# Performance work log

Measured on AMD Instinct MI355X. Metric: run time of the kernel, lower is better.

The kernel has to match this reference:

```python
import jax, jax.numpy as jnp
import numpy as np

B, S = 2, 2048
H = 16
NOPE, ROPE, VD = 128, 64, 128
Q_RANK, KV_RANK = 1536, 512
SCALE = 1.0 / np.sqrt(NOPE + ROPE)  # 1/sqrt(192)
NEG_INF = -10000.0


def _make_rope(n_pos, dim):
    # matches gen_rope: theta over even indices, angles repeated twice (rotate-half layout)
    theta = 1.0 / (10000.0 ** (np.arange(0, dim, 2, dtype=np.float32) / dim))
    pos = np.arange(n_pos, dtype=np.float32)
    ang = np.outer(pos, theta)                      # [N, dim/2]
    ang = np.concatenate([ang, ang], axis=-1)       # [N, dim]
    return jnp.asarray(np.cos(ang)), jnp.asarray(np.sin(ang))


def _rope(x, cos, sin):
    # rotate-half RoPE; cos/sin broadcast over head dim if present
    d = x.shape[-1]
    x1, x2 = x[..., : d // 2], x[..., d // 2 :]
    rot = jnp.concatenate([-x2, x1], axis=-1)
    return x * cos + rot * sin


def setup_inputs() -> dict:
    key = jax.random.key(0)
    ks = jax.random.split(key, 5)
    Q = jax.random.normal(ks[0], (B, S, Q_RANK), dtype=jnp.float32)
    KV = jax.random.normal(ks[1], (B, S, KV_RANK), dtype=jnp.float32)
    PE = jax.random.normal(ks[2], (B, S, ROPE), dtype=jnp.float32)
    WUQ = jax.random.normal(ks[3], (H * (NOPE + ROPE), Q_RANK), dtype=jnp.float32) * 0.02
    WUKV = jax.random.normal(ks[4], (H * (NOPE + VD), KV_RANK), dtype=jnp.float32) * 0.02
    cos, sin = _make_rope(B * S, ROPE)
    cos = cos.reshape(B, S, ROPE)
    sin = sin.reshape(B, S, ROPE)
    mask = jnp.triu(jnp.full((S, S), NEG_INF, dtype=jnp.float32), k=1)
    return {"Q": Q, "KV": KV, "PE": PE, "WUQ": WUQ, "WUKV": WUKV,
            "cos": cos, "sin": sin, "mask": mask}


def reference(Q, KV, PE, WUQ, WUKV, cos, sin, mask):
    b, s, _ = Q.shape
    # low-rank up-projections
    q = jnp.einsum("bsl,dl->bsd", Q, WUQ).reshape(b, s, H, NOPE + ROPE)
    q_nope, q_pe = q[..., :NOPE], q[..., NOPE:]
    q_pe = _rope(q_pe, cos[:, :, None, :], sin[:, :, None, :])

    kv = jnp.einsum("bsl,dl->bsd", KV, WUKV).reshape(b, s, H, NOPE + VD)
    k_nope, v = kv[..., :NOPE], kv[..., NOPE:]
    k_pe = _rope(PE, cos, sin)  # [b, s, ROPE], shared across heads

    # attention scores: per-head nope part + shared rope part
    scores = jnp.einsum("bqhd,bkhd->bhqk", q_nope, k_nope)
    scores = scores + jnp.einsum("bqhd,bkd->bhqk", q_pe, k_pe)
    scores = scores * SCALE + mask[None, None, :, :]
    attn = jax.nn.softmax(scores, axis=-1)
    out = jnp.einsum("bhqk,bkhd->bqhd", attn, v)  # [b, s, H, VD]
    return out
```

## Files before the change

### kernel.cpp

```cpp
#include <hip/hip_runtime.h>

typedef __attribute__((ext_vector_type(8))) short short8;
typedef __attribute__((ext_vector_type(4))) float f32x4;

#define SS 2048
#define HH 16
#define NOPE_D 128
#define ROPE_D 64
#define VDIM 128
#define QD 192
#define SCALE_F 0.07216878364870323f
#define LOG2E 1.4426950408889634f

__device__ __forceinline__ unsigned short f2bf(float f) {
    unsigned int x = __builtin_bit_cast(unsigned int, f);
    unsigned int r = (x + 0x7fffu + ((x >> 16) & 1u)) >> 16;
    return (unsigned short)r;
}

#define GLDS16(g, l) __builtin_amdgcn_global_load_lds( \
    (const __attribute__((address_space(1))) void*)(g), \
    (__attribute__((address_space(3))) void*)(l), 16, 0, 0)

__global__ __launch_bounds__(256) void cvt_all(
    const float* __restrict__ Q, const float* __restrict__ WUQ,
    const float* __restrict__ KV, const float* __restrict__ WUKV,
    const float* __restrict__ PE, const float* __restrict__ cs, const float* __restrict__ sn,
    unsigned short* __restrict__ Qb, unsigned short* __restrict__ WUQb,
    unsigned short* __restrict__ KVb, unsigned short* __restrict__ WUKVb,
    unsigned short* __restrict__ kpe)
{
    int bid = blockIdx.x;
    if (bid >= 14848) {
        int idx = (bid - 14848) * 256 + threadIdx.x;
        int i = idx & 31, row = idx >> 5;
        float x1 = PE[row * 64 + i], x2 = PE[row * 64 + 32 + i];
        float c1 = cs[row * 64 + i],      s1 = sn[row * 64 + i];
        float c2 = cs[row * 64 + 32 + i], s2 = sn[row * 64 + 32 + i];
        kpe[row * 64 + i]      = f2bf(x1 * c1 - x2 * s1);
        kpe[row * 64 + 32 + i] = f2bf(x2 * c2 + x1 * s2);
        return;
    }
    const float* src; unsigned short* dst; float scale = 1.0f;
    if (bid < 6144)       { src = Q;    dst = Qb; }
    else if (bid < 10752) { src = WUQ;  dst = WUQb; bid -= 6144; scale = SCALE_F * LOG2E; }
    else if (bid < 12800) { src = KV;   dst = KVb;  bid -= 10752; }
    else                  { src = WUKV; dst = WUKVb; bid -= 12800; }
    int i = (bid * 256 + threadIdx.x) * 4;
    float4 v = *(const float4*)(src + i);
    ushort4 o = { f2bf(v.x * scale), f2bf(v.y * scale), f2bf(v.z * scale), f2bf(v.w * scale) };
    *(ushort4*)(dst + i) = o;
}

__global__ __launch_bounds__(256) void gemm_fused(
    const unsigned short* __restrict__ Qb, const unsigned short* __restrict__ WUQb,
    const unsigned short* __restrict__ KVb, const unsigned short* __restrict__ WUKVb,
    unsigned short* __restrict__ qbuf, unsigned short* __restrict__ knope,
    unsigned short* __restrict__ vT,
    const float* __restrict__ cs, const float* __restrict__ sn)
{
    __shared__ unsigned short As[128 * 64];
    __shared__ unsigned short Bs[128 * 64];
    const int t = threadIdx.x, w = t >> 6, lane = t & 63;
    const int n16 = lane & 15, quad = lane >> 4;

    int bid = blockIdx.x;
    const unsigned short *A, *B; int N, K, bm, bn; bool g1;
    if (bid < 768) { g1 = true;  A = Qb;  B = WUQb;  N = 3072; K = 1536;
                     bm = (bid / 24) * 128; bn = (bid % 24) * 128; }
    else           { g1 = false; bid -= 768; A = KVb; B = WUKVb; N = 4096; K = 512;
                     bm = (bid / 32) * 128; bn = (bid % 32) * 128; }

    const int wm = (w >> 1) * 64, wn = (w & 1) * 64;
    f32x4 acc[4][4] = {};

    const int lr = lane >> 3, lc = lane & 7;
    const int sw = (lc ^ lr) * 8;
    const unsigned short* gA = A + (size_t)(bm + w * 32 + lr) * K + sw;
    const unsigned short* gB = B + (size_t)(bn + w * 32 + lr) * K + sw;

    for (int k0 = 0; k0 < K; k0 += 64) {
        __syncthreads();
        for (int j = 0; j < 4; j++) {
            GLDS16(gA + (size_t)j * 8 * K + k0, &As[(w * 32 + j * 8) * 64]);
            GLDS16(gB + (size_t)j * 8 * K + k0, &Bs[(w * 32 + j * 8) * 64]);
        }
        __syncthreads();
        for (int ks = 0; ks < 2; ks++) {
            short8 af[4], bf[4];
            for (int mt = 0; mt < 4; mt++) {
                int rw = wm + mt * 16 + n16;
                af[mt] = *(const short8*)&As[rw * 64 + (((ks * 4 + quad) ^ (rw & 7)) * 8)];
            }
            for (int nt = 0; nt < 4; nt++) {
                int rw = wn + nt * 16 + n16;
                bf[nt] = *(const short8*)&Bs[rw * 64 + (((ks * 4 + quad) ^ (rw & 7)) * 8)];
            }
            for (int mt = 0; mt < 4; mt++)
                for (int nt = 0; nt < 4; nt++)
                    acc[mt][nt] = __builtin_amdgcn_mfma_f32_16x16x32_bf16(af[mt], bf[nt], acc[mt][nt], 0, 0, 0);
        }
    }

    const int colbase = bn + wn;
    if (g1) {
        const bool is_pe = ((colbase % 192) >= 128);
        if (is_pe) {
            for (int mt = 0; mt < 4; mt++)
                for (int r = 0; r < 4; r++) {
                    int row = bm + wm + mt * 16 + quad * 4 + r;
                    const float* cr = cs + row * 64;
                    const float* sr = sn + row * 64;
                    for (int nt = 0; nt < 2; nt++) {
                        int i = nt * 16 + n16;
                        float x1 = acc[mt][nt][r], x2 = acc[mt][nt + 2][r];
                        float o1 = x1 * cr[i] - x2 * sr[i];
                        float o2 = x2 * cr[32 + i] + x1 * sr[32 + i];
                        qbuf[(size_t)row * N + colbase + i] = f2bf(o1);
                        qbuf[(size_t)row * N + colbase + 32 + i] = f2bf(o2);
                    }
                }
        } else {
            for (int mt = 0; mt < 4; mt++)
                for (int nt = 0; nt < 4; nt++)
                    for (int r = 0; r < 4; r++)
                        qbuf[(size_t)(bm + wm + mt * 16 + quad * 4 + r) * N + colbase + nt * 16 + n16]
                            = f2bf(acc[mt][nt][r]);
        }
    } else {
        if ((colbase & 255) < 128) {
            for (int mt = 0; mt < 4; mt++)
                for (int nt = 0; nt < 4; nt++) {
                    int col = colbase + nt * 16 + n16;
                    int h = col >> 8, d = col & 255;
                    for (int r = 0; r < 4; r++)
                        knope[(size_t)(bm + wm + mt * 16 + quad * 4 + r) * 2048 + h * 128 + d]
                            = f2bf(acc[mt][nt][r]);
                }
        } else {
            for (int mt = 0; mt < 4; mt++)
                for (int nt = 0; nt < 4; nt++) {
                    int col = colbase + nt * 16 + n16;
                    int h = col >> 8, vd = (col & 255) - 128;
                    int row0 = bm + wm + mt * 16 + quad * 4;
                    int b = row0 >> 11, s0 = row0 & 2047;
                    int l6 = s0 & 63;
                    int scol = (s0 & ~63) + ((l6 >> 5) & 1) * 32 + ((l6 >> 2) & 3) * 8
                             + ((l6 >> 4) & 1) * 4 + (l6 & 3);
                    ushort4 pk = { f2bf(acc[mt][nt][0]), f2bf(acc[mt][nt][1]),
                                   f2bf(acc[mt][nt][2]), f2bf(acc[mt][nt][3]) };
                    *(ushort4*)&vT[((size_t)(b * 16 + h) * 128 + vd) * 2048 + scol] = pk;
                }
        }
    }
}

#define STAGE(bufsel, kt_) do { \
    int r_ = w * 16 + (lane >> 4), sl_ = lane & 15; \
    for (int j = 0; j < 4; j++) { \
        int rr_ = r_ + j * 4; \
        GLDS16(knb + (size_t)((kt_) * 64 + rr_) * 2048 + ((sl_ ^ (rr_ & 7)) * 8), \
               &Kn[bufsel][(w * 16 + j * 4) * 128]); \
    } \
    int rp_ = w * 16 + (lane >> 3), slp_ = lane & 7; \
    for (int j = 0; j < 2; j++) { \
        int rr_ = rp_ + j * 8; \
        GLDS16(kpb + (size_t)((kt_) * 64 + rr_) * 64 + ((slp_ ^ (rr_ & 7)) * 8), \
               &Kp[bufsel][(w * 16 + j * 8) * 64]); \
    } \
    int r2_ = w * 32 + (lane >> 3), sl2_ = lane & 7; \
    for (int j = 0; j < 4; j++) { \
        int rr_ = r2_ + j * 8; \
        GLDS16(vtb + (size_t)rr_ * 2048 + (kt_) * 64 + ((sl2_ ^ (rr_ & 7)) * 8), \
               &Vt[bufsel][(w * 32 + j * 8) * 64]); \
    } \
} while (0)

#define COMPUTE(bufsel, kt_) do { \
    f32x4 Sg[2][4]; \
    __builtin_amdgcn_s_setprio(1); \
    for (int nt = 0; nt < 4; nt++) { \
        int key = nt * 16 + n16, kx = key & 7; \
        f32x4 a0 = {}, a1 = {}; \
        for (int ks = 0; ks < 4; ks++) { \
            short8 af = *(const short8*)&Kn[bufsel][key * 128 + (((ks * 4 + quad) ^ kx) * 8)]; \
            a0 = __builtin_amdgcn_mfma_f32_16x16x32_bf16(af, qf[0][ks], a0, 0, 0, 0); \
            a1 = __builtin_amdgcn_mfma_f32_16x16x32_bf16(af, qf[1][ks], a1, 0, 0, 0); \
        } \
        for (int ks = 0; ks < 2; ks++) { \
            short8 af = *(const short8*)&Kp[bufsel][key * 64 + (((ks * 4 + quad) ^ kx) * 8)]; \
            a0 = __builtin_amdgcn_mfma_f32_16x16x32_bf16(af, qf[0][4 + ks], a0, 0, 0, 0); \
            a1 = __builtin_amdgcn_mfma_f32_16x16x32_bf16(af, qf[1][4 + ks], a1, 0, 0, 0); \
        } \
        Sg[0][nt] = a0; Sg[1][nt] = a1; \
    } \
    __builtin_amdgcn_s_setprio(0); \
    if ((kt_) >= 2 * qt) {    \
        for (int qg = 0; qg < 2; qg++) { \
            int qq = qt * 128 + w * 32 + qg * 16 + n16; \
            for (int nt = 0; nt < 4; nt++) { \
                int key0 = (kt_) * 64 + nt * 16 + quad * 4; \
                for (int r = 0; r < 4; r++) \
                    if (key0 + r > qq) Sg[qg][nt][r] = -INFINITY; \
            } \
        } \
    } \
     \
    float alpha[2]; \
    for (int qg = 0; qg < 2; qg++) { \
        float mx = -INFINITY; \
        for (int nt = 0; nt < 4; nt++) \
            for (int r = 0; r < 4; r++) mx = fmaxf(mx, Sg[qg][nt][r]); \
        mx = fmaxf(mx, __shfl_xor(mx, 16, 64)); \
        mx = fmaxf(mx, __shfl_xor(mx, 32, 64)); \
        float mnew = fmaxf(m_i[qg], mx); \
        alpha[qg] = exp2f(m_i[qg] - mnew); \
        m_i[qg] = mnew; \
        float rs = 0.f; \
        for (int nt = 0; nt < 4; nt++) \
            for (int r = 0; r < 4; r++) { \
                float pv = exp2f(Sg[qg][nt][r] - mnew); \
                Sg[qg][nt][r] = pv; \
                rs += pv; \
            } \
        l_i[qg] = l_i[qg] * alpha[qg] + rs; \
    } \
     \
     \
    f32x4 av0, av1; \
    for (int r_ = 0; r_ < 4; r_++) { \
        av0[r_] = __shfl(alpha[0], quad * 4 + r_, 64); \
        av1[r_] = __shfl(alpha[1], quad * 4 + r_, 64); \
    } \
    for (int v8 = 0; v8 < 8; v8++) \
        for (int r = 0; r < 4; r++) { \
            O[0][v8][r] *= av0[r]; \
            O[1][v8][r] *= av1[r]; \
        } \
     \
    short8 pp[2][2]; \
    for (int qg = 0; qg < 2; qg++) \
        for (int ntp = 0; ntp < 2; ntp++) { \
            short8 pa; \
            for (int j = 0; j < 4; j++) pa[j] = (short)f2bf(Sg[qg][ntp * 2][j]); \
            for (int j = 0; j < 4; j++) pa[4 + j] = (short)f2bf(Sg[qg][ntp * 2 + 1][j]); \
            pp[qg][ntp] = pa; \
        } \
    __builtin_amdgcn_s_setprio(1); \
    for (int ntp = 0; ntp < 2; ntp++) \
        for (int v8 = 0; v8 < 8; v8++) { \
            int vd = v8 * 16 + n16; \
            short8 vb = *(const short8*)&Vt[bufsel][vd * 64 + (((ntp * 4 + quad) ^ (vd & 7)) * 8)]; \
            O[0][v8] = __builtin_amdgcn_mfma_f32_16x16x32_bf16(pp[0][ntp], vb, O[0][v8], 0, 0, 0); \
            O[1][v8] = __builtin_amdgcn_mfma_f32_16x16x32_bf16(pp[1][ntp], vb, O[1][v8], 0, 0, 0); \
        } \
    __builtin_amdgcn_s_setprio(0); \
} while (0)

__global__ __launch_bounds__(256, 2) void attn_kernel(
    const unsigned short* __restrict__ qbuf,
    const unsigned short* __restrict__ knope,
    const unsigned short* __restrict__ kpe,
    const unsigned short* __restrict__ vT,
    float* __restrict__ out)
{
    const int t = threadIdx.x, w = t >> 6, lane = t & 63;
    const int n16 = lane & 15, quad = lane >> 4;

    __shared__ unsigned short Kn[2][64 * 128];
    __shared__ unsigned short Kp[2][64 * 64];
    __shared__ unsigned short Vt[2][128 * 64];

    const int u = blockIdx.x;
    const int sbits = (u >> 1) & 15;
    const int flip  = (u & 1) ^ ((u >> 8) & 1);
    const int qt = flip ? 15 - sbits : sbits;
    const int c  = ((u >> 5) & 7) | ((u & 1) << 3) | (((u >> 8) & 1) << 4);
    const int h = c & 15, b = c >> 4;

    const unsigned short* knb = knope + (size_t)b * 2048 * 2048 + h * 128;
    const unsigned short* kpb = kpe + (size_t)b * 2048 * 64;
    const unsigned short* vtb = vT + (size_t)(b * 16 + h) * 128 * 2048;

    short8 qf[2][6];
    for (int qg = 0; qg < 2; qg++) {
        size_t grow = (size_t)(b * SS + qt * 128 + w * 32 + qg * 16 + n16);
        const unsigned short* qp = qbuf + grow * (HH * QD) + h * QD + quad * 8;
        for (int ks = 0; ks < 6; ks++) qf[qg][ks] = *(const short8*)(qp + ks * 32);
    }

    f32x4 O[2][8] = {};
    float m_i[2] = { -INFINITY, -INFINITY };
    float l_i[2] = { 0.f, 0.f };

    const int nkt = 2 * qt + 2;

    STAGE(0, 0);
    __syncthreads();
    for (int kt2 = 0; kt2 < nkt; kt2 += 2) {
        STAGE(1, kt2 + 1);
        COMPUTE(0, kt2);
        __syncthreads();
        if (kt2 + 2 < nkt) STAGE(0, kt2 + 2);
        COMPUTE(1, kt2 + 1);
        __syncthreads();
    }

    float l0 = l_i[0];
    l0 += __shfl_xor(l0, 16, 64); l0 += __shfl_xor(l0, 32, 64);
    float l1 = l_i[1];
    l1 += __shfl_xor(l1, 16, 64); l1 += __shfl_xor(l1, 32, 64);
    float rl0 = 1.f / l0, rl1 = 1.f / l1;
    f32x4 lv0, lv1;
    for (int r_ = 0; r_ < 4; r_++) {
        lv0[r_] = __shfl(rl0, quad * 4 + r_, 64);
        lv1[r_] = __shfl(rl1, quad * 4 + r_, 64);
    }
    for (int qg = 0; qg < 2; qg++) {
        const f32x4 lv = qg ? lv1 : lv0;
        for (int r = 0; r < 4; r++) {
            size_t qrow = (size_t)(b * SS + qt * 128 + w * 32 + qg * 16 + quad * 4 + r);
            float* op = out + (qrow * HH + h) * VDIM;
            for (int v8 = 0; v8 < 8; v8++)
                op[v8 * 16 + n16] = O[qg][v8][r] * lv[r];
        }
    }
}

extern "C" void kernel_launch(void* const* d_in, const int* in_sizes, int n_in,
                              void* d_out, int out_size, void* d_ws, size_t ws_size,
                              hipStream_t stream) {
    const float* Q    = (const float*)d_in[0];
    const float* KV   = (const float*)d_in[1];
    const float* PE   = (const float*)d_in[2];
    const float* WUQ  = (const float*)d_in[3];
    const float* WUKV = (const float*)d_in[4];
    const float* cosp = (const float*)d_in[5];
    const float* sinp = (const float*)d_in[6];
    float* out = (float*)d_out;

    unsigned short* qbuf  = (unsigned short*)d_ws;
    unsigned short* knope = qbuf  + (size_t)4096 * 3072;
    unsigned short* vT    = knope + (size_t)4096 * 2048;
    unsigned short* kpe   = vT    + (size_t)4096 * 2048;
    unsigned short* Qb    = kpe   + (size_t)4096 * 64;
    unsigned short* WUQb  = Qb    + (size_t)4096 * 1536;
    unsigned short* KVb   = WUQb  + (size_t)3072 * 1536;
    unsigned short* WUKVb = KVb   + (size_t)4096 * 512;

    cvt_all<<<15360, 256, 0, stream>>>(Q, WUQ, KV, WUKV, PE, cosp, sinp,
                                       Qb, WUQb, KVb, WUKVb, kpe);
    gemm_fused<<<1792, 256, 0, stream>>>(Qb, WUQb, KVb, WUKVb,
                                         qbuf, knope, vT, cosp, sinp);
    attn_kernel<<<512, 256, 0, stream>>>(qbuf, knope, kpe, vT, out);
}
```

Measured before the change: 345.8 us.

## Use partial vmcnt waits, lazy softmax rescaling, and drop setprio and occupancy hint

Replaces the full __syncthreads barriers with explicit s_waitcnt vmcnt(10)/lgkmcnt(0) plus s_barrier, so the next tile's global-to-LDS loads can stay in flight while the current tile is computed. Adds a lazy online-softmax rescale: when every lane's new row max exceeds the running max by at most 8 (log2 domain), the max is not updated and the O rescale is skipped. Also removes the s_setprio hints and the min-blocks-per-CU launch bound. The hand-counted vmcnt(10) must match the number of outstanding loads per STAGE exactly, and the lazy max lets exponent values grow up to 2^8 before renormalising.

```diff
diff --git a/kernel.cpp b/kernel.cpp
--- a/kernel.cpp
+++ b/kernel.cpp
@@ -178,7 +178,6 @@
 
 #define COMPUTE(bufsel, kt_) do { \
     f32x4 Sg[2][4]; \
-    __builtin_amdgcn_s_setprio(1); \
     for (int nt = 0; nt < 4; nt++) { \
         int key = nt * 16 + n16, kx = key & 7; \
         f32x4 a0 = {}, a1 = {}; \
@@ -194,7 +193,6 @@
         } \
         Sg[0][nt] = a0; Sg[1][nt] = a1; \
     } \
-    __builtin_amdgcn_s_setprio(0); \
     if ((kt_) >= 2 * qt) {    \
         for (int qg = 0; qg < 2; qg++) { \
             int qq = qt * 128 + w * 32 + qg * 16 + n16; \
@@ -207,14 +205,17 @@
     } \
      \
     float alpha[2]; \
+    bool skipq[2]; \
     for (int qg = 0; qg < 2; qg++) { \
         float mx = -INFINITY; \
         for (int nt = 0; nt < 4; nt++) \
             for (int r = 0; r < 4; r++) mx = fmaxf(mx, Sg[qg][nt][r]); \
         mx = fmaxf(mx, __shfl_xor(mx, 16, 64)); \
         mx = fmaxf(mx, __shfl_xor(mx, 32, 64)); \
-        float mnew = fmaxf(m_i[qg], mx); \
-        alpha[qg] = exp2f(m_i[qg] - mnew); \
+        const bool skip = __all(mx - m_i[qg] <= 8.0f); \
+        skipq[qg] = skip; \
+        float mnew = skip ? m_i[qg] : fmaxf(m_i[qg], mx); \
+        alpha[qg] = skip ? 1.0f : exp2f(m_i[qg] - mnew); \
         m_i[qg] = mnew; \
         float rs = 0.f; \
         for (int nt = 0; nt < 4; nt++) \
@@ -226,17 +227,18 @@
         l_i[qg] = l_i[qg] * alpha[qg] + rs; \
     } \
      \
-     \
-    f32x4 av0, av1; \
-    for (int r_ = 0; r_ < 4; r_++) { \
-        av0[r_] = __shfl(alpha[0], quad * 4 + r_, 64); \
-        av1[r_] = __shfl(alpha[1], quad * 4 + r_, 64); \
-    } \
-    for (int v8 = 0; v8 < 8; v8++) \
-        for (int r = 0; r < 4; r++) { \
-            O[0][v8][r] *= av0[r]; \
-            O[1][v8][r] *= av1[r]; \
-        } \
+    if (!skipq[0]) { \
+        f32x4 av0; \
+        for (int r_ = 0; r_ < 4; r_++) av0[r_] = __shfl(alpha[0], quad * 4 + r_, 64); \
+        for (int v8 = 0; v8 < 8; v8++) \
+            for (int r = 0; r < 4; r++) O[0][v8][r] *= av0[r]; \
+    } \
+    if (!skipq[1]) { \
+        f32x4 av1; \
+        for (int r_ = 0; r_ < 4; r_++) av1[r_] = __shfl(alpha[1], quad * 4 + r_, 64); \
+        for (int v8 = 0; v8 < 8; v8++) \
+            for (int r = 0; r < 4; r++) O[1][v8][r] *= av1[r]; \
+    } \
      \
     short8 pp[2][2]; \
     for (int qg = 0; qg < 2; qg++) \
@@ -246,7 +248,6 @@
             for (int j = 0; j < 4; j++) pa[4 + j] = (short)f2bf(Sg[qg][ntp * 2 + 1][j]); \
             pp[qg][ntp] = pa; \
         } \
-    __builtin_amdgcn_s_setprio(1); \
     for (int ntp = 0; ntp < 2; ntp++) \
         for (int v8 = 0; v8 < 8; v8++) { \
             int vd = v8 * 16 + n16; \
@@ -254,10 +255,19 @@
             O[0][v8] = __builtin_amdgcn_mfma_f32_16x16x32_bf16(pp[0][ntp], vb, O[0][v8], 0, 0, 0); \
             O[1][v8] = __builtin_amdgcn_mfma_f32_16x16x32_bf16(pp[1][ntp], vb, O[1][v8], 0, 0, 0); \
         } \
-    __builtin_amdgcn_s_setprio(0); \
 } while (0)
 
-__global__ __launch_bounds__(256, 2) void attn_kernel(
+#define WAIT_VM10  do { asm volatile("s_waitcnt vmcnt(10)" ::: "memory"); \
+                        __builtin_amdgcn_sched_barrier(0); \
+                        __builtin_amdgcn_s_barrier(); } while (0)
+#define WAIT_VM0   do { asm volatile("s_waitcnt vmcnt(0)" ::: "memory"); \
+                        __builtin_amdgcn_sched_barrier(0); \
+                        __builtin_amdgcn_s_barrier(); } while (0)
+#define RELEASE    do { asm volatile("s_waitcnt lgkmcnt(0)" ::: "memory"); \
+                        __builtin_amdgcn_sched_barrier(0); \
+                        __builtin_amdgcn_s_barrier(); } while (0)
+
+__global__ __launch_bounds__(256) void attn_kernel(
     const unsigned short* __restrict__ qbuf,
     const unsigned short* __restrict__ knope,
     const unsigned short* __restrict__ kpe,
@@ -296,14 +306,19 @@
     const int nkt = 2 * qt + 2;
 
     STAGE(0, 0);
-    __syncthreads();
     for (int kt2 = 0; kt2 < nkt; kt2 += 2) {
         STAGE(1, kt2 + 1);
+        WAIT_VM10;
         COMPUTE(0, kt2);
-        __syncthreads();
-        if (kt2 + 2 < nkt) STAGE(0, kt2 + 2);
+        RELEASE;
+        if (kt2 + 2 < nkt) {
+            STAGE(0, kt2 + 2);
+            WAIT_VM10;
+        } else {
+            WAIT_VM0;
+        }
         COMPUTE(1, kt2 + 1);
-        __syncthreads();
+        RELEASE;
     }
 
     float l0 = l_i[0];
```

Result: no change. 348.0 us (+0.6%).
